# Kernel tuning notes

Hardware: AMD Instinct MI355X
Metric: run time of the kernel (lower is better)

Reference implementation:

```python
import jax, jax.numpy as jnp
import numpy as np
from jax import lax

B, C_IN, C_OUT, H, W, E = 16, 256, 256, 32, 32, 8


def setup_inputs() -> dict:
    key = jax.random.key(0)
    k = jax.random.split(key, 5)
    x = jax.random.normal(k[0], (B, C_IN, H, W), dtype=jnp.float32)
    # router: Conv2d(C_IN, E, kernel_size=1) -> weight [E, C_IN], bias [E]
    wc = jax.random.normal(k[1], (E, C_IN), dtype=jnp.float32) / np.sqrt(C_IN)
    bc = jnp.zeros((E,), dtype=jnp.float32)
    # experts: E x Conv2d(C_IN, C_OUT, 3, padding=1) + ReLU
    we = jax.random.normal(k[2], (E, C_OUT, C_IN, 3, 3), dtype=jnp.float32) / np.sqrt(C_IN * 9)
    be = jnp.zeros((E, C_OUT), dtype=jnp.float32)
    return {"x": x, "wc": wc, "bc": bc, "we": we, "be": be}


def reference(x, wc, bc, we, be):
    Bx = x.shape[0]
    # controller: 1x1 conv then global avg-pool == pool then linear
    pooled = jnp.mean(x, axis=(2, 3))                      # [B, C_IN]
    logits = pooled @ wc.T + bc                            # [B, E]
    decisions = jnp.argmax(logits, axis=1)                 # [B] int
    # run ALL experts on the full batch as one grouped conv: weight [E*C_OUT, C_IN, 3, 3]
    w_all = we.reshape(E * C_OUT, C_IN, 3, 3)
    y = lax.conv_general_dilated(
        x, w_all, window_strides=(1, 1), padding="SAME",
        dimension_numbers=("NCHW", "OIHW", "NCHW"))        # [B, E*C_OUT, H, W]
    y = y + be.reshape(1, E * C_OUT, 1, 1)
    y = jax.nn.relu(y).reshape(Bx, E, C_OUT, H, W)
    # faithful to forward_test: out block i is components[dec[i]](x) for the FULL batch
    # out[i*B + j] = y[j, dec[i]]
    gathered = y[:, decisions]                             # [j, i, C_OUT, H, W]
    out = jnp.swapaxes(gathered, 0, 1).reshape(Bx * Bx, C_OUT, H, W)
    return out
```

## Files before the change

### kernel.cpp

```cpp
#include <hip/hip_runtime.h>
#include <hip/hip_bf16.h>
#include <stdint.h>

#define B_    16
#define CIN   256
#define COUT  256
#define E_    8
#define HW    1024

typedef __attribute__((ext_vector_type(8))) short  short8;
typedef __attribute__((ext_vector_type(4))) float  floatx4;

#define XT_OFF 17408
#define WT_OFF (XT_OFF + B_*HW*CIN*2)

__global__ void pool_kernel(const float* __restrict__ x, float* __restrict__ pooled) {
    int b = blockIdx.x, c = blockIdx.y;
    const float4* p = (const float4*)(x + ((size_t)b*CIN + c)*HW);
    int t = threadIdx.x;
    float4 v = p[t];
    float s = v.x + v.y + v.z + v.w;
    #pragma unroll
    for (int o = 32; o > 0; o >>= 1) s += __shfl_down(s, o, 64);
    __shared__ float wsum[4];
    if ((t & 63) == 0) wsum[t >> 6] = s;
    __syncthreads();
    if (t == 0) pooled[b*CIN + c] = (wsum[0]+wsum[1]+wsum[2]+wsum[3]) * (1.0f/1024.0f);
}

__global__ void decide_kernel(const float* __restrict__ pooled, const float* __restrict__ wc,
                              const float* __restrict__ bc, int* __restrict__ dec) {
    int t = threadIdx.x;
    int b = t >> 3, e = t & 7;
    float acc = bc[e];
    const float* pp = pooled + b*CIN;
    const float* ww = wc + e*CIN;
    for (int i = 0; i < CIN; ++i) acc += pp[i] * ww[i];
    __shared__ float lg[16][8];
    lg[b][e] = acc;
    __syncthreads();
    if (e == 0) {
        float best = lg[b][0]; int bi = 0;
        #pragma unroll
        for (int j = 1; j < 8; ++j) { if (lg[b][j] > best) { best = lg[b][j]; bi = j; } }
        dec[b] = bi;
    }
}

__global__ void xpose_kernel(const float* __restrict__ x, unsigned short* __restrict__ xt) {
    int b = blockIdx.x;
    int hw0 = blockIdx.y * 32;
    int ci0 = blockIdx.z * 32;
    __shared__ float tile[32][33];
    int t = threadIdx.x;
    int j = t & 31;
    int i = t >> 5;
    #pragma unroll
    for (int p = 0; p < 4; ++p)
        tile[i + p*8][j] = x[((size_t)b*CIN + ci0 + i + p*8)*HW + hw0 + j];
    __syncthreads();
    int cw = t & 31;
    int rw = t >> 5;
    #pragma unroll
    for (int p = 0; p < 4; ++p) {
        int hw = hw0 + rw + p*8;
        __hip_bfloat16 h = __float2bfloat16(tile[cw][rw + p*8]);
        xt[((size_t)b*HW + hw)*CIN + ci0 + cw] = *(unsigned short*)&h;
    }
}

__global__ void wpose_kernel(const float* __restrict__ we, unsigned short* __restrict__ wt) {
    int ec = blockIdx.x;
    int e = ec >> 8, co = ec & 255;
    int ci = threadIdx.x;
    const float* src = we + (((size_t)e*COUT + co)*CIN + ci)*9;
    #pragma unroll
    for (int rs = 0; rs < 9; ++rs) {
        __hip_bfloat16 h = __float2bfloat16(src[rs]);
        wt[(((size_t)e*9 + rs)*COUT + co)*CIN + ci] = *(unsigned short*)&h;
    }
}

__global__ __launch_bounds__(256) void conv_kernel(
    const unsigned short* __restrict__ xt, const unsigned short* __restrict__ wt,
    const float* __restrict__ be, const int* __restrict__ dec,
    float* __restrict__ out) {

    int tile = blockIdx.x;
    int b = blockIdx.y;
    int e = blockIdx.z;
    int mt = tile >> 3, nt = tile & 7;

    int dcs[16];
    #pragma unroll
    for (int i = 0; i < 16; ++i) dcs[i] = dec[i];
    bool active = false;
    #pragma unroll
    for (int i = 0; i < 16; ++i) active |= (dcs[i] == e);
    if (!active) return;

    __shared__ __align__(16) unsigned short sA[128*32];
    __shared__ __align__(16) unsigned short sB[6*34*32];

    int t = threadIdx.x;
    int wave = t >> 6, lane = t & 63;
    int wm = wave >> 1, wn = wave & 1;
    int kg = lane >> 4, ln = lane & 15;

    int h0  = nt * 4;
    int co0 = mt * 128;

    floatx4 acc[4][4];
    #pragma unroll
    for (int i = 0; i < 4; ++i)
        #pragma unroll
        for (int j = 0; j < 4; ++j) acc[i][j] = (floatx4)0.0f;

    const unsigned short* xb = xt + (size_t)b*HW*CIN;

    for (int ck = 0; ck < 8; ++ck) {
        int ci0 = ck * 32;
        for (int c = t; c < 816; c += 256) {
            int ci16 = c & 3;
            int col  = (c >> 2) % 34;
            int row  = c / 136;
            int gh = h0 - 1 + row;
            int gw = col - 1;
            uint4 v = make_uint4(0u, 0u, 0u, 0u);
            if (gh >= 0 && gh < 32 && gw >= 0 && gw < 32)
                v = *(const uint4*)(xb + ((size_t)gh*32 + gw)*CIN + ci0 + ci16*8);
            *(uint4*)(&sB[(row*34 + col)*32 + ci16*8]) = v;
        }
        for (int sh = 0; sh < 9; ++sh) {
            const unsigned short* wsrc = wt + (((size_t)e*9 + sh)*COUT + co0)*CIN + ci0;
            {
                int rowA = t >> 2;
                int cip  = (t & 3) * 8;
                *(uint4*)(&sA[rowA*32 + cip])      = *(const uint4*)(wsrc + (size_t)rowA*CIN + cip);
                *(uint4*)(&sA[(rowA+64)*32 + cip]) = *(const uint4*)(wsrc + (size_t)(rowA+64)*CIN + cip);
            }
            __syncthreads();

            short8 a[4], bb[4];
            #pragma unroll
            for (int im = 0; im < 4; ++im)
                a[im] = *(const short8*)(&sA[(wm*64 + im*16 + ln)*32 + kg*8]);
            int r = sh / 3, s = sh % 3;
            #pragma unroll
            for (int in = 0; in < 4; ++in) {
                int n  = wn*64 + in*16 + ln;
                int hl = n >> 5, wl = n & 31;
                bb[in] = *(const short8*)(&sB[((hl + r)*34 + (wl + s))*32 + kg*8]);
            }
            __syncthreads();

            #pragma unroll
            for (int im = 0; im < 4; ++im)
                #pragma unroll
                for (int in = 0; in < 4; ++in)
                    acc[im][in] = __builtin_amdgcn_mfma_f32_16x16x32_bf16(a[im], bb[in], acc[im][in], 0, 0, 0);
        }
    }

    #pragma unroll
    for (int im = 0; im < 4; ++im) {
        int co = co0 + wm*64 + im*16 + kg*4;
        #pragma unroll
        for (int rg = 0; rg < 4; ++rg) {
            float bv = be[e*COUT + co + rg];
            #pragma unroll
            for (int in = 0; in < 4; ++in) {
                float v = acc[im][in][rg] + bv;
                acc[im][in][rg] = v > 0.0f ? v : 0.0f;
            }
        }
    }
    for (int i = 0; i < 16; ++i) {
        if (dcs[i] != e) continue;
        float* ob = out + (size_t)(i*16 + b)*COUT*HW;
        #pragma unroll
        for (int im = 0; im < 4; ++im) {
            int co = co0 + wm*64 + im*16 + kg*4;
            #pragma unroll
            for (int in = 0; in < 4; ++in) {
                int hw = nt*128 + wn*64 + in*16 + ln;
                #pragma unroll
                for (int rg = 0; rg < 4; ++rg)
                    ob[(size_t)(co + rg)*HW + hw] = acc[im][in][rg];
            }
        }
    }
}

extern "C" void kernel_launch(void* const* d_in, const int* in_sizes, int n_in,
                              void* d_out, int out_size, void* d_ws, size_t ws_size,
                              hipStream_t stream) {
    const float* x  = (const float*)d_in[0];
    const float* wc = (const float*)d_in[1];
    const float* bc = (const float*)d_in[2];
    const float* we = (const float*)d_in[3];
    const float* be = (const float*)d_in[4];
    float* out = (float*)d_out;

    char* ws = (char*)d_ws;
    int*   dec    = (int*)ws;
    float* pooled = (float*)(ws + 64);
    unsigned short* xt = (unsigned short*)(ws + XT_OFF);
    unsigned short* wt = (unsigned short*)(ws + WT_OFF);

    pool_kernel  <<<dim3(16, 256), 256, 0, stream>>>(x, pooled);
    decide_kernel<<<1, 128, 0, stream>>>(pooled, wc, bc, dec);
    xpose_kernel <<<dim3(16, 32, 8), 256, 0, stream>>>(x, xt);
    wpose_kernel <<<2048, 256, 0, stream>>>(we, wt);
    conv_kernel  <<<dim3(16, 16, 8), 256, 0, stream>>>(xt, wt, be, dec, out);
}
```

Before: 496.5 us.

## Pre-pad transposed input and use direct global-to-LDS loads in conv

```diff
diff --git a/kernel.cpp b/kernel.cpp
--- a/kernel.cpp
+++ b/kernel.cpp
@@ -7,12 +7,22 @@
 #define COUT  256
 #define E_    8
 #define HW    1024
+#define PH    34
+#define PW    34
 
 typedef __attribute__((ext_vector_type(8))) short  short8;
 typedef __attribute__((ext_vector_type(4))) float  floatx4;
 
 #define XT_OFF 17408
-#define WT_OFF (XT_OFF + B_*HW*CIN*2)
+#define XT_BYTES (B_*PH*PW*CIN*2)
+#define WT_OFF (XT_OFF + XT_BYTES)
+
+__device__ __forceinline__ void gld_lds16(const void* g, void* l) {
+    __builtin_amdgcn_global_load_lds(
+        (const __attribute__((address_space(1))) unsigned int*)g,
+        (__attribute__((address_space(3))) unsigned int*)l,
+        16, 0, 0);
+}
 
 __global__ void pool_kernel(const float* __restrict__ x, float* __restrict__ pooled) {
     int b = blockIdx.x, c = blockIdx.y;
@@ -33,9 +43,13 @@
     int t = threadIdx.x;
     int b = t >> 3, e = t & 7;
     float acc = bc[e];
-    const float* pp = pooled + b*CIN;
-    const float* ww = wc + e*CIN;
-    for (int i = 0; i < CIN; ++i) acc += pp[i] * ww[i];
+    const float4* pp = (const float4*)(pooled + b*CIN);
+    const float4* ww = (const float4*)(wc + e*CIN);
+    #pragma unroll 4
+    for (int i = 0; i < CIN/4; ++i) {
+        float4 p = pp[i], w = ww[i];
+        acc += p.x*w.x + p.y*w.y + p.z*w.z + p.w*w.w;
+    }
     __shared__ float lg[16][8];
     lg[b][e] = acc;
     __syncthreads();
@@ -64,20 +78,24 @@
     #pragma unroll
     for (int p = 0; p < 4; ++p) {
         int hw = hw0 + rw + p*8;
-        __hip_bfloat16 h = __float2bfloat16(tile[cw][rw + p*8]);
-        xt[((size_t)b*HW + hw)*CIN + ci0 + cw] = *(unsigned short*)&h;
+        int h = hw >> 5, w = hw & 31;
+        __hip_bfloat16 hv = __float2bfloat16(tile[cw][rw + p*8]);
+        xt[(((size_t)b*PH + h + 1)*PW + (w + 1))*CIN + ci0 + cw] = *(unsigned short*)&hv;
     }
 }
 
 __global__ void wpose_kernel(const float* __restrict__ we, unsigned short* __restrict__ wt) {
-    int ec = blockIdx.x;
-    int e = ec >> 8, co = ec & 255;
-    int ci = threadIdx.x;
-    const float* src = we + (((size_t)e*COUT + co)*CIN + ci)*9;
+    int e = blockIdx.x >> 8, co = blockIdx.x & 255;
+    __shared__ float buf[CIN*9];
+    const float* src = we + ((size_t)e*COUT + co)*CIN*9;
+    int t = threadIdx.x;
+    #pragma unroll
+    for (int k = 0; k < 9; ++k) buf[t + k*256] = src[t + k*256];
+    __syncthreads();
     #pragma unroll
     for (int rs = 0; rs < 9; ++rs) {
-        __hip_bfloat16 h = __float2bfloat16(src[rs]);
-        wt[(((size_t)e*9 + rs)*COUT + co)*CIN + ci] = *(unsigned short*)&h;
+        __hip_bfloat16 h = __float2bfloat16(buf[t*9 + rs]);
+        wt[(((size_t)e*9 + rs)*COUT + co)*CIN + t] = *(unsigned short*)&h;
     }
 }
 
@@ -99,15 +117,15 @@
     for (int i = 0; i < 16; ++i) active |= (dcs[i] == e);
     if (!active) return;
 
-    __shared__ __align__(16) unsigned short sA[128*32];
-    __shared__ __align__(16) unsigned short sB[6*34*32];
+    __shared__ __align__(16) unsigned short sA[512*8];
+    __shared__ __align__(16) unsigned short sB[1024*8];
 
     int t = threadIdx.x;
     int wave = t >> 6, lane = t & 63;
     int wm = wave >> 1, wn = wave & 1;
     int kg = lane >> 4, ln = lane & 15;
 
-    int h0  = nt * 4;
+    int ph0 = nt * 4;
     int co0 = mt * 128;
 
     floatx4 acc[4][4];
@@ -116,41 +134,40 @@
         #pragma unroll
         for (int j = 0; j < 4; ++j) acc[i][j] = (floatx4)0.0f;
 
-    const unsigned short* xb = xt + (size_t)b*HW*CIN;
+    const unsigned short* xb = xt + (size_t)b*PH*PW*CIN;
 
     for (int ck = 0; ck < 8; ++ck) {
         int ci0 = ck * 32;
-        for (int c = t; c < 816; c += 256) {
-            int ci16 = c & 3;
-            int col  = (c >> 2) % 34;
-            int row  = c / 136;
-            int gh = h0 - 1 + row;
-            int gw = col - 1;
-            uint4 v = make_uint4(0u, 0u, 0u, 0u);
-            if (gh >= 0 && gh < 32 && gw >= 0 && gw < 32)
-                v = *(const uint4*)(xb + ((size_t)gh*32 + gw)*CIN + ci0 + ci16*8);
-            *(uint4*)(&sB[(row*34 + col)*32 + ci16*8]) = v;
+        #pragma unroll
+        for (int k = 0; k < 4; ++k) {
+            int c = t + k*256;
+            int cc = c < 816 ? c : 815;
+            int row = cc / 136;
+            int rem = cc - row*136;
+            int col = rem >> 2;
+            int g   = rem & 3;
+            gld_lds16(xb + ((size_t)(ph0 + row)*PW + col)*CIN + ci0 + g*8, &sB[c*8]);
         }
         for (int sh = 0; sh < 9; ++sh) {
             const unsigned short* wsrc = wt + (((size_t)e*9 + sh)*COUT + co0)*CIN + ci0;
-            {
-                int rowA = t >> 2;
-                int cip  = (t & 3) * 8;
-                *(uint4*)(&sA[rowA*32 + cip])      = *(const uint4*)(wsrc + (size_t)rowA*CIN + cip);
-                *(uint4*)(&sA[(rowA+64)*32 + cip]) = *(const uint4*)(wsrc + (size_t)(rowA+64)*CIN + cip);
+            #pragma unroll
+            for (int k = 0; k < 2; ++k) {
+                int c = t + k*256;
+                int rowA = c >> 2, g = c & 3;
+                gld_lds16(wsrc + (size_t)rowA*CIN + g*8, &sA[c*8]);
             }
             __syncthreads();
 
             short8 a[4], bb[4];
             #pragma unroll
             for (int im = 0; im < 4; ++im)
-                a[im] = *(const short8*)(&sA[(wm*64 + im*16 + ln)*32 + kg*8]);
-            int r = sh / 3, s = sh % 3;
+                a[im] = *(const short8*)(&sA[((wm*64 + im*16 + ln)*4 + kg)*8]);
+            int r = sh / 3, s = sh - r*3;
             #pragma unroll
             for (int in = 0; in < 4; ++in) {
                 int n  = wn*64 + in*16 + ln;
                 int hl = n >> 5, wl = n & 31;
-                bb[in] = *(const short8*)(&sB[((hl + r)*34 + (wl + s))*32 + kg*8]);
+                bb[in] = *(const short8*)(&sB[(((hl + r)*34 + (wl + s))*4 + kg)*8]);
             }
             __syncthreads();
 
@@ -208,6 +225,8 @@
     unsigned short* xt = (unsigned short*)(ws + XT_OFF);
     unsigned short* wt = (unsigned short*)(ws + WT_OFF);
 
+    hipMemsetAsync(xt, 0, XT_BYTES, stream);
+
     pool_kernel  <<<dim3(16, 256), 256, 0, stream>>>(x, pooled);
     decide_kernel<<<1, 128, 0, stream>>>(pooled, wc, bc, dec);
     xpose_kernel <<<dim3(16, 32, 8), 256, 0, stream>>>(x, xt);
```

After: 469.2 us. 5.5% less time.
